# Kernel tuning notes

Measured on AMD Instinct MI355X. Metric: run time of the kernel, lower is better.

Reference implementation:

```python
import jax, jax.numpy as jnp
import numpy as np

B, CIN, CCTX, K, V, T, KS = 8, 512, 512, 64, 256, 1024, 23
EPS = 1e-5


def _bn(z, gamma, beta):
    # train-mode BatchNorm1d over (batch, time) per channel, biased variance
    mean = jnp.mean(z, axis=(0, 2), keepdims=True)
    var = jnp.mean((z - mean) ** 2, axis=(0, 2), keepdims=True)
    return (z - mean) * jax.lax.rsqrt(var + EPS) * gamma[None, :, None] + beta[None, :, None]


def setup_inputs() -> dict:
    key = jax.random.key(0)
    ks = jax.random.split(key, 10)
    x = jax.random.normal(ks[0], (B, CIN, T), dtype=jnp.float32)
    context = jax.random.normal(ks[1], (B, CCTX, T), dtype=jnp.float32)
    Wq = jax.random.normal(ks[2], (K, CIN), dtype=jnp.float32) * (CIN ** -0.5)
    bq = jnp.zeros((K,), dtype=jnp.float32)
    Wk = jax.random.normal(ks[3], (K, CCTX), dtype=jnp.float32) * (CCTX ** -0.5)
    bk = jnp.zeros((K,), dtype=jnp.float32)
    Wv = jax.random.normal(ks[4], (V, CCTX), dtype=jnp.float32) * (CCTX ** -0.5)
    bv = jnp.zeros((V,), dtype=jnp.float32)
    gamma_q = jnp.ones((K,), dtype=jnp.float32)
    beta_q = jnp.zeros((K,), dtype=jnp.float32)
    gamma_v = jnp.ones((V,), dtype=jnp.float32)
    beta_v = jnp.zeros((V,), dtype=jnp.float32)
    pos_w = jax.random.normal(ks[5], (K, KS), dtype=jnp.float32) * (KS ** -0.5)
    pos_b = jnp.zeros((K,), dtype=jnp.float32)
    return {"x": x, "context": context, "Wq": Wq, "bq": bq, "Wk": Wk, "bk": bk,
            "Wv": Wv, "bv": bv, "gamma_q": gamma_q, "beta_q": beta_q,
            "gamma_v": gamma_v, "beta_v": beta_v, "pos_w": pos_w, "pos_b": pos_b}


def reference(x, context, Wq, bq, Wk, bk, Wv, bv,
              gamma_q, beta_q, gamma_v, beta_v, pos_w, pos_b):
    # 1x1 conv1d == channel matmul
    queries = jnp.einsum('bct,kc->bkt', x, Wq) + bq[None, :, None]          # (B,K,T)
    keys = jnp.einsum('bct,kc->bkt', context, Wk) + bk[None, :, None]       # (B,K,T)
    values = jnp.einsum('bct,vc->bvt', context, Wv) + bv[None, :, None]     # (B,V,T)

    norm_keys = jax.nn.softmax(keys, axis=-1)                               # softmax over T
    queries = _bn(queries, gamma_q, beta_q)
    values = _bn(values, gamma_v, beta_v)

    q_t = jnp.transpose(queries, (0, 2, 1))                                 # (B,T,K)
    v_t = jnp.transpose(values, (0, 2, 1))                                  # (B,T,V)

    content_lambda = jnp.einsum('bkt,btv->bkv', norm_keys, v_t)             # (B,K,V)

    # positional conv2d: kernel (K,1,KS,1), padding (KS//2, 0) along T
    lhs = v_t[:, None, :, :]                                                # (B,1,T,V)
    rhs = pos_w[:, None, :, None]                                           # (K,1,KS,1)
    pl = jax.lax.conv_general_dilated(
        lhs, rhs, window_strides=(1, 1),
        padding=[(KS // 2, KS // 2), (0, 0)],
        dimension_numbers=('NCHW', 'OIHW', 'NCHW'))
    pl = pl + pos_b[None, :, None, None]                                    # (B,K,T,V)
    pl = jnp.transpose(pl, (0, 2, 1, 3))                                    # (B,T,K,V)

    content_out = jnp.einsum('btk,bkv->btv', q_t, content_lambda)           # (B,T,V)
    positional_out = jnp.einsum('btk,btkv->btv', q_t, pl)                   # (B,T,V)

    return jnp.transpose(content_out + positional_out, (0, 2, 1))           # (B,V,T)
```

## Files before the change

kernel.cpp:

```cpp
#include <hip/hip_runtime.h>
#include <math.h>

#define B_ 8
#define CIN_ 512
#define K_ 64
#define V_ 256
#define T_ 1024
#define KS_ 23
#define EPS_ 1e-5f
#define NTC_ 8

typedef __attribute__((ext_vector_type(8))) short bf16x8;
typedef __attribute__((ext_vector_type(4))) float f32x4;

__device__ __forceinline__ unsigned short f2bf(float f) {
    union { float f; unsigned u; } x; x.f = f;
    unsigned r = x.u + 0x7fffu + ((x.u >> 16) & 1u);
    return (unsigned short)(r >> 16);
}
__device__ __forceinline__ float bf2f(unsigned short h) {
    union { unsigned u; float f; } x; x.u = ((unsigned)h) << 16;
    return x.f;
}

__device__ __forceinline__ void gload16(const unsigned short* g, unsigned short* l) {
    __builtin_amdgcn_global_load_lds(
        (const __attribute__((address_space(1))) unsigned int*)(const void*)g,
        (__attribute__((address_space(3))) unsigned int*)(void*)l, 16, 0, 0);
}

__global__ __launch_bounds__(256) void prep_kernel(
    const float* __restrict__ x, const float* __restrict__ ctx,
    const float* __restrict__ Wq, const float* __restrict__ Wk,
    const float* __restrict__ Wv,
    unsigned short* __restrict__ xT, unsigned short* __restrict__ cT,
    unsigned short* __restrict__ Wb, float* __restrict__ stat)
{
    __shared__ unsigned short sh[64][72];
    const int tid = threadIdx.x;
    const int id = blockIdx.x;
    if (id < 2048) {
        const int t0 = (id & 15) * 64, c0 = ((id >> 4) & 7) * 64;
        const int z = id >> 7, b = z & 7, which = z >> 3;
        const float* src = which ? ctx : x;
        unsigned short* dst = which ? cT : xT;
        const int cl = tid >> 2, qq = tid & 3;
        const float* row = src + ((size_t)b * CIN_ + c0 + cl) * T_ + t0 + qq * 16;
        #pragma unroll
        for (int u = 0; u < 4; u++) {
            float4 f = *(const float4*)(row + 4 * u);
            sh[qq * 16 + 4 * u + 0][cl] = f2bf(f.x);
            sh[qq * 16 + 4 * u + 1][cl] = f2bf(f.y);
            sh[qq * 16 + 4 * u + 2][cl] = f2bf(f.z);
            sh[qq * 16 + 4 * u + 3][cl] = f2bf(f.w);
        }
        __syncthreads();
        const int tl = tid >> 2;
        unsigned short* orow = dst + ((size_t)b * T_ + t0 + tl) * CIN_ + c0 + qq * 16;
        *(bf16x8*)(orow)     = *(bf16x8*)&sh[tl][qq * 16];
        *(bf16x8*)(orow + 8) = *(bf16x8*)&sh[tl][qq * 16 + 8];
    } else {
        const int wid = id - 2048;
        if (wid == 0) {
            #pragma unroll
            for (int i = 0; i < 3; i++) {
                int idx = tid + i * 256;
                if (idx < 672) ((float4*)stat)[idx] = make_float4(0.f, 0.f, 0.f, 0.f);
            }
        }
        const int i4 = wid * 256 + tid;
        const int n1 = K_ * CIN_ / 4, n2 = 2 * K_ * CIN_ / 4;
        const float* src; int off;
        if (i4 < n1)      { src = Wq; off = i4; }
        else if (i4 < n2) { src = Wk; off = i4 - n1; }
        else              { src = Wv; off = i4 - n2; }
        float4 f = ((const float4*)src)[off];
        ushort4 h;
        h.x = f2bf(f.x); h.y = f2bf(f.y); h.z = f2bf(f.z); h.w = f2bf(f.w);
        *(ushort4*)(Wb + (size_t)i4 * 4) = h;
    }
}

__global__ __launch_bounds__(256) void proj_mfma6(
    const unsigned short* __restrict__ xT, const unsigned short* __restrict__ cT,
    const unsigned short* __restrict__ Wb,
    const float* __restrict__ bq, const float* __restrict__ bk,
    const float* __restrict__ bv,
    float* __restrict__ k_buf, float* __restrict__ v_raw,
    unsigned short* __restrict__ qT, float* __restrict__ stat,
    float* __restrict__ kml)
{
    __shared__ __align__(16) unsigned short SMb[2][12288];

    const int tid = threadIdx.x;
    const int b = blockIdx.z, t0 = blockIdx.x * 128, yb = blockIdx.y;

    const unsigned short* in; const unsigned short* W; const float* bias;
    float* outp = nullptr; int ch0 = 0; float* ssum = nullptr; float* ssq = nullptr;
    if (yb == 0)      { in = xT; W = Wb;             bias = bq;
                        ssum = stat; ssq = stat + 64; ch0 = 0; }
    else if (yb == 1) { in = cT; W = Wb + K_ * CIN_; bias = bk;
                        outp = k_buf + (size_t)b * K_ * T_; }
    else { int m0 = (yb - 2) * 64; in = cT;
           W = Wb + 2 * K_ * CIN_ + (size_t)m0 * CIN_; bias = bv + m0;
           outp = v_raw + ((size_t)b * V_ + m0) * T_;
           ssum = stat + 128; ssq = stat + 384; ch0 = m0; }

    const int lane = tid & 63, w = tid >> 6;
    const int col = lane & 15, quad = lane >> 4;

    const int gW0 = (0 * 4 + w) * 64 + lane, rW0 = gW0 >> 3;
    const int gW1 = (1 * 4 + w) * 64 + lane, rW1 = gW1 >> 3;
    const unsigned short* sW0 = W + (size_t)rW0 * CIN_ + (((gW0 & 7) ^ (rW0 & 7)) * 8);
    const unsigned short* sW1 = W + (size_t)rW1 * CIN_ + (((gW1 & 7) ^ (rW1 & 7)) * 8);

    const int gX0 = (0 * 4 + w) * 64 + lane, rX0 = gX0 >> 3;
    const int gX1 = (1 * 4 + w) * 64 + lane, rX1 = gX1 >> 3;
    const int gX2 = (2 * 4 + w) * 64 + lane, rX2 = gX2 >> 3;
    const int gX3 = (3 * 4 + w) * 64 + lane, rX3 = gX3 >> 3;
    const size_t xbase = (size_t)b * T_ + t0;
    const unsigned short* sX0 = in + (xbase + rX0) * CIN_ + (((gX0 & 7) ^ (rX0 & 7)) * 8);
    const unsigned short* sX1 = in + (xbase + rX1) * CIN_ + (((gX1 & 7) ^ (rX1 & 7)) * 8);
    const unsigned short* sX2 = in + (xbase + rX2) * CIN_ + (((gX2 & 7) ^ (rX2 & 7)) * 8);
    const unsigned short* sX3 = in + (xbase + rX3) * CIN_ + (((gX3 & 7) ^ (rX3 & 7)) * 8);

#define STAGE(P, C0) do { \
    unsigned short* Wt_ = SMb[P]; \
    unsigned short* Xt_ = SMb[P] + 4096; \
    gload16(sW0 + (C0), Wt_ + w * 512); \
    gload16(sW1 + (C0), Wt_ + 2048 + w * 512); \
    gload16(sX0 + (C0), Xt_ + w * 512); \
    gload16(sX1 + (C0), Xt_ + 2048 + w * 512); \
    gload16(sX2 + (C0), Xt_ + 4096 + w * 512); \
    gload16(sX3 + (C0), Xt_ + 6144 + w * 512); \
} while (0)

    f32x4 acc[8];
    #pragma unroll
    for (int j = 0; j < 8; j++) acc[j] = (f32x4){0.f, 0.f, 0.f, 0.f};

    STAGE(0, 0);
    for (int s = 0; s < 8; s++) {
        const int cur = s & 1;
        if (s < 7) {
            STAGE(cur ^ 1, (s + 1) * 64);
            asm volatile("s_waitcnt vmcnt(6)" ::: "memory");
        } else {
            asm volatile("s_waitcnt vmcnt(0)" ::: "memory");
        }
        __builtin_amdgcn_s_barrier();
        __builtin_amdgcn_sched_barrier(0);
        {
            const unsigned short* Wt = SMb[cur];
            const unsigned short* Xt = SMb[cur] + 4096;
            #pragma unroll
            for (int ks = 0; ks < 2; ks++) {
                const int kc = ((ks * 4 + quad) ^ (col & 7)) * 8;
                bf16x8 af = *(bf16x8*)&Wt[(w * 16 + col) * 64 + kc];
                #pragma unroll
                for (int j = 0; j < 8; j++) {
                    bf16x8 bfr = *(bf16x8*)&Xt[(j * 16 + col) * 64 + kc];
                    acc[j] = __builtin_amdgcn_mfma_f32_16x16x32_bf16(af, bfr, acc[j], 0, 0, 0);
                }
            }
        }
        __builtin_amdgcn_sched_barrier(0);
        __builtin_amdgcn_s_barrier();
    }
#undef STAGE

    float bias_v[4], s_[4], sq[4], mr[4], lr[4];
    #pragma unroll
    for (int r = 0; r < 4; r++) {
        bias_v[r] = bias[w * 16 + quad * 4 + r];
        s_[r] = 0.f; sq[r] = 0.f; mr[r] = -1e30f; lr[r] = 0.f;
    }
    unsigned short* SE = SMb[0];
    #pragma unroll
    for (int j = 0; j < 8; j++) {
        float o[4];
        #pragma unroll
        for (int r = 0; r < 4; r++) {
            o[r] = acc[j][r] + bias_v[r];
            s_[r] += o[r]; sq[r] += o[r] * o[r];
        }
        if (yb == 0) {
            ushort4 h;
            h.x = f2bf(o[0]); h.y = f2bf(o[1]); h.z = f2bf(o[2]); h.w = f2bf(o[3]);
            *(ushort4*)&SE[(j * 16 + col) * 72 + w * 16 + quad * 4] = h;
        } else {
            #pragma unroll
            for (int r = 0; r < 4; r++)
                outp[(size_t)(w * 16 + quad * 4 + r) * T_ + t0 + j * 16 + col] = o[r];
            if (yb == 1) {
                #pragma unroll
                for (int r = 0; r < 4; r++) {
                    float mn = fmaxf(mr[r], o[r]);
                    lr[r] = lr[r] * __expf(mr[r] - mn) + __expf(o[r] - mn);
                    mr[r] = mn;
                }
            }
        }
    }
    if (yb == 0) {
        __syncthreads();
        const int tr = tid >> 1, h2 = tid & 1;
        unsigned short* dq = qT + ((size_t)b * T_ + t0 + tr) * K_ + h2 * 32;
        #pragma unroll
        for (int u = 0; u < 4; u++)
            *(bf16x8*)(dq + u * 8) = *(bf16x8*)&SE[tr * 72 + h2 * 32 + u * 8];
    }
    if (yb == 1) {
        #pragma unroll
        for (int r = 0; r < 4; r++) {
            float m = mr[r], l = lr[r];
            #pragma unroll
            for (int off = 1; off < 16; off <<= 1) {
                float mo = __shfl_xor(m, off, 64);
                float lo = __shfl_xor(l, off, 64);
                float mn = fmaxf(m, mo);
                l = l * __expf(m - mn) + lo * __expf(mo - mn);
                m = mn;
            }
            if (col == 0) {
                int row = w * 16 + quad * 4 + r;
                float* p = kml + (((size_t)b * K_ + row) * 8 + (t0 >> 7)) * 2;
                p[0] = m; p[1] = l;
            }
        }
    } else {
        #pragma unroll
        for (int r = 0; r < 4; r++) {
            float sv = s_[r], qv = sq[r];
            #pragma unroll
            for (int off = 1; off < 16; off <<= 1) {
                sv += __shfl_xor(sv, off, 64);
                qv += __shfl_xor(qv, off, 64);
            }
            if (col == 0) {
                int ch = ch0 + w * 16 + quad * 4 + r;
                atomicAdd(&ssum[ch], sv);
                atomicAdd(&ssq[ch], qv);
            }
        }
    }
}

__global__ __launch_bounds__(256) void lambda_kernel5(
    const float* __restrict__ k_buf, const float* __restrict__ v_raw,
    const float* __restrict__ kml, float* __restrict__ clp)
{
    __shared__ __align__(16) float nks[K_][68];
    __shared__ __align__(16) float vls[64][68];
    __shared__ float mrow[64], lrow[64];
    const int tid = threadIdx.x;
    const int b = blockIdx.z, v0 = blockIdx.y * 64, tc = blockIdx.x;

    if (tid < 64) {
        const float2* p = (const float2*)(kml + ((size_t)b * K_ + tid) * 16);
        float m = -1e30f, l = 0.f;
        #pragma unroll
        for (int sgi = 0; sgi < 8; sgi++) {
            float2 ml = p[sgi];
            float mn = fmaxf(m, ml.x);
            l = l * __expf(m - mn) + ml.y * __expf(ml.x - mn);
            m = mn;
        }
        mrow[tid] = m; lrow[tid] = 1.f / l;
    }
    __syncthreads();

    const int r = tid >> 2, q = tid & 3;
    const int tv = tid & 15, tk = tid >> 4;
    float4 acc[4];
    #pragma unroll
    for (int i = 0; i < 4; i++) acc[i] = make_float4(0.f, 0.f, 0.f, 0.f);

    for (int c2 = 0; c2 < 2; c2++) {
        const int t0 = (tc * 2 + c2) * 64;
        if (c2) __syncthreads();
        {
            const float* nrow = k_buf + ((size_t)b * K_ + r) * T_ + t0;
            const float* vrow = v_raw + ((size_t)b * V_ + v0 + r) * T_ + t0;
            const float mr = mrow[r], li = lrow[r];
            #pragma unroll
            for (int i = 0; i < 4; i++) {
                int c4 = q + 4 * i;
                float4 g = *(const float4*)(nrow + 4 * c4);
                g.x = __expf(g.x - mr) * li; g.y = __expf(g.y - mr) * li;
                g.z = __expf(g.z - mr) * li; g.w = __expf(g.w - mr) * li;
                *(float4*)&nks[r][4 * c4] = g;
                float4 h = *(const float4*)(vrow + 4 * c4);
                vls[4 * c4 + 0][r] = h.x; vls[4 * c4 + 1][r] = h.y;
                vls[4 * c4 + 2][r] = h.z; vls[4 * c4 + 3][r] = h.w;
            }
        }
        __syncthreads();
        for (int tt = 0; tt < 16; tt++) {
            float4 w0 = *(float4*)&vls[4 * tt + 0][4 * tv];
            float4 w1 = *(float4*)&vls[4 * tt + 1][4 * tv];
            float4 w2 = *(float4*)&vls[4 * tt + 2][4 * tv];
            float4 w3 = *(float4*)&vls[4 * tt + 3][4 * tv];
            #pragma unroll
            for (int i = 0; i < 4; i++) {
                float4 n = *(float4*)&nks[4 * tk + i][4 * tt];
                acc[i] += w0 * n.x + w1 * n.y + w2 * n.z + w3 * n.w;
            }
        }
    }
    #pragma unroll
    for (int i = 0; i < 4; i++)
        *(float4*)&clp[(((size_t)b * NTC_ + tc) * K_ + 4 * tk + i) * V_ + v0 + 4 * tv] = acc[i];
}

__global__ __launch_bounds__(256) void prep_cl_kernel3(
    const float* __restrict__ clp, const float* __restrict__ stat,
    const float* __restrict__ gq, const float* __restrict__ betaq,
    const float* __restrict__ gv, const float* __restrict__ betav,
    unsigned short* __restrict__ clb2, float* __restrict__ hterm)
{
    __shared__ float qsc[64], qsh[64], red[4][64];
    const int tid = threadIdx.x;
    const int b = blockIdx.y, v0 = blockIdx.x * 64, kz = blockIdx.z;
    const float inv_n = 1.f / (B_ * T_);
    if (tid < 64) {
        float mean = stat[tid] * inv_n;
        float var  = stat[64 + tid] * inv_n - mean * mean;
        float sc = gq[tid] * rsqrtf(var + EPS_);
        qsc[tid] = sc; qsh[tid] = betaq[tid] - mean * sc;
    }
    const int vl = tid & 63, kq = tid >> 6;
    const int c = v0 + vl;
    float vmean = stat[128 + c] * inv_n;
    float vvar  = stat[384 + c] * inv_n - vmean * vmean;
    float vsv = gv[c] * rsqrtf(vvar + EPS_);
    float vhv = betav[c] - vmean * vsv;
    __syncthreads();
    float h = 0.f;
    #pragma unroll
    for (int kk = 0; kk < 4; kk++) {
        int k = kz * 16 + kq * 4 + kk;
        float a = 0.f;
        #pragma unroll
        for (int tc = 0; tc < NTC_; tc++)
            a += clp[(((size_t)b * NTC_ + tc) * K_ + k) * V_ + c];
        float clbv = a * vsv + vhv;
        h += qsh[k] * clbv;
        clb2[((size_t)b * V_ + c) * K_ + k] = f2bf(clbv * qsc[k]);
    }
    red[kq][vl] = h;
    __syncthreads();
    if (tid < 64)
        atomicAdd(&hterm[(size_t)b * V_ + v0 + tid],
                  red[0][tid] + red[1][tid] + red[2][tid] + red[3][tid]);
}

__global__ __launch_bounds__(256) void out_kernel5(
    const unsigned short* __restrict__ qT, const unsigned short* __restrict__ clb2,
    const float* __restrict__ hterm, const float* __restrict__ v_raw,
    const float* __restrict__ stat,
    const float* __restrict__ gq, const float* __restrict__ betaq,
    const float* __restrict__ gv, const float* __restrict__ betav,
    const float* __restrict__ pos_w, const float* __restrict__ pos_b,
    float* __restrict__ out)
{
    __shared__ unsigned short qTt[64][72];
    __shared__ unsigned short clv[64][72];
    __shared__ float vs2T[88][68];
    __shared__ float qpt[64][28];
    __shared__ float pws[64][24];
    __shared__ float qsc[64], qsh[64];
    __shared__ float consts[24];
    __shared__ float hvs[64];
    const int tid = threadIdx.x;
    const int b = blockIdx.z, v0 = blockIdx.y * 64, t0 = blockIdx.x * 64;
    const float inv_n = 1.f / (B_ * T_);

    if (tid < 64) {
        float mean = stat[tid] * inv_n;
        float var  = stat[64 + tid] * inv_n - mean * mean;
        float sc = gq[tid] * rsqrtf(var + EPS_);
        qsc[tid] = sc; qsh[tid] = betaq[tid] - mean * sc;
        hvs[tid] = hterm[(size_t)b * V_ + v0 + tid];
    }
    {
        const int rl = tid >> 2, part = tid & 3;
        const unsigned short* qs = qT + ((size_t)b * T_ + t0 + rl) * K_ + part * 16;
        *(bf16x8*)&qTt[rl][part * 16]     = *(const bf16x8*)(qs);
        *(bf16x8*)&qTt[rl][part * 16 + 8] = *(const bf16x8*)(qs + 8);
        const unsigned short* cs = clb2 + ((size_t)b * V_ + v0 + rl) * K_ + part * 16;
        *(bf16x8*)&clv[rl][part * 16]     = *(const bf16x8*)(cs);
        *(bf16x8*)&clv[rl][part * 16 + 8] = *(const bf16x8*)(cs + 8);
    }
    {
        const int vl = tid >> 2, qq = tid & 3;
        const int c = v0 + vl;
        float vmean = stat[128 + c] * inv_n;
        float vvar  = stat[384 + c] * inv_n - vmean * vmean;
        float vsv = gv[c] * rsqrtf(vvar + EPS_);
        float vhv = betav[c] - vmean * vsv;
        const float* vrow = v_raw + ((size_t)b * V_ + c) * T_;
        #pragma unroll
        for (int i = 0; i < 22; i++) {
            int cc = qq + 4 * i;
            if (cc < 86) {
                int t = t0 + cc - 11;
                vs2T[cc][vl] = (t >= 0 && t < T_) ? vrow[t] * vsv + vhv : 0.f;
            }
        }
    }
    __syncthreads();

    for (int idx = tid; idx < K_ * 24; idx += 256) {
        int k = idx / 24, s = idx % 24;
        pws[k][s] = qsc[k] * (s < KS_ ? pos_w[k * KS_ + s] : pos_b[k]);
    }
    if (tid < 24) {
        float cs = 0.f;
        for (int k = 0; k < K_; k++)
            cs += qsh[k] * (tid < KS_ ? pos_w[k * KS_ + tid] : pos_b[k]);
        consts[tid] = cs;
    }
    __syncthreads();

    {
        const int t = tid >> 2, sg = tid & 3, s0 = sg * 6;
        float a[6];
        #pragma unroll
        for (int u = 0; u < 6; u++) a[u] = consts[s0 + u];
        #pragma unroll
        for (int kb = 0; kb < 8; kb++) {
            bf16x8 qv = *(bf16x8*)&qTt[t][kb * 8];
            #pragma unroll
            for (int j = 0; j < 8; j++) {
                float q = bf2f((unsigned short)qv[j]);
                #pragma unroll
                for (int u = 0; u < 6; u++) a[u] += q * pws[kb * 8 + j][s0 + u];
            }
        }
        #pragma unroll
        for (int u = 0; u < 6; u++) qpt[t][s0 + u] = a[u];
    }
    __syncthreads();

    const int lane = tid & 63, w = tid >> 6;
    const int col = lane & 15, quad = lane >> 4;

    f32x4 acc[4];
    #pragma unroll
    for (int tf = 0; tf < 4; tf++) acc[tf] = (f32x4){0.f, 0.f, 0.f, 0.f};

    #pragma unroll
    for (int ks = 0; ks < 2; ks++) {
        const int kc = ks * 32 + quad * 8;
        bf16x8 af = *(bf16x8*)&clv[w * 16 + col][kc];
        #pragma unroll
        for (int tf = 0; tf < 4; tf++) {
            bf16x8 bq = *(bf16x8*)&qTt[tf * 16 + col][kc];
            acc[tf] = __builtin_amdgcn_mfma_f32_16x16x32_bf16(af, bq, acc[tf], 0, 0, 0);
        }
    }

    const int vb = w * 16 + quad * 4;
    float4 hv4 = *(float4*)&hvs[vb];
    #pragma unroll
    for (int tf = 0; tf < 4; tf++) {
        const int lt = tf * 16 + col;
        float qv[24];
        #pragma unroll
        for (int u = 0; u < 6; u++)
            *(float4*)&qv[4 * u] = *(float4*)&qpt[lt][4 * u];
        float4 a; a.x = acc[tf][0]; a.y = acc[tf][1]; a.z = acc[tf][2]; a.w = acc[tf][3];
        #pragma unroll
        for (int s = 0; s < KS_; s++) {
            float4 wv = *(float4*)&vs2T[lt + s][vb];
            a.x += qv[s] * wv.x; a.y += qv[s] * wv.y;
            a.z += qv[s] * wv.z; a.w += qv[s] * wv.w;
        }
        float base = qv[23];
        a.x += base + hv4.x; a.y += base + hv4.y;
        a.z += base + hv4.z; a.w += base + hv4.w;
        float* ap = (float*)&a;
        #pragma unroll
        for (int r = 0; r < 4; r++)
            out[((size_t)b * V_ + v0 + vb + r) * T_ + t0 + lt] = ap[r];
    }
}

extern "C" void kernel_launch(void* const* d_in, const int* in_sizes, int n_in,
                              void* d_out, int out_size, void* d_ws, size_t ws_size,
                              hipStream_t stream)
{
    const float* x     = (const float*)d_in[0];
    const float* ctx   = (const float*)d_in[1];
    const float* Wq    = (const float*)d_in[2];
    const float* bq    = (const float*)d_in[3];
    const float* Wk    = (const float*)d_in[4];
    const float* bk    = (const float*)d_in[5];
    const float* Wv    = (const float*)d_in[6];
    const float* bv    = (const float*)d_in[7];
    const float* gq    = (const float*)d_in[8];
    const float* betaq = (const float*)d_in[9];
    const float* gv    = (const float*)d_in[10];
    const float* betav = (const float*)d_in[11];
    const float* pos_w = (const float*)d_in[12];
    const float* pos_b = (const float*)d_in[13];
    float* out = (float*)d_out;

    float* ws    = (float*)d_ws;
    float* k_buf = ws;
    float* v_raw = k_buf + (size_t)B_ * K_ * T_;
    float* clp   = v_raw + (size_t)B_ * V_ * T_;
    float* stat  = clp + (size_t)B_ * NTC_ * K_ * V_;
    float* hterm = stat + 640;
    float* kml   = hterm + (size_t)B_ * V_;
    unsigned short* xT   = (unsigned short*)(kml + (size_t)B_ * K_ * 16);
    unsigned short* cT   = xT + (size_t)B_ * T_ * CIN_;
    unsigned short* Wb   = cT + (size_t)B_ * T_ * CIN_;
    unsigned short* qT   = Wb + (size_t)(2 * K_ + V_) * CIN_;
    unsigned short* clb2 = qT + (size_t)B_ * T_ * K_;

    prep_kernel<<<dim3(2048 + 192), 256, 0, stream>>>(
        x, ctx, Wq, Wk, Wv, xT, cT, Wb, stat);
    proj_mfma6<<<dim3(T_ / 128, 6, B_), 256, 0, stream>>>(
        xT, cT, Wb, bq, bk, bv, k_buf, v_raw, qT, stat, kml);
    lambda_kernel5<<<dim3(NTC_, V_ / 64, B_), 256, 0, stream>>>(k_buf, v_raw, kml, clp);
    prep_cl_kernel3<<<dim3(V_ / 64, B_, 4), 256, 0, stream>>>(
        clp, stat, gq, betaq, gv, betav, clb2, hterm);
    out_kernel5<<<dim3(T_ / 64, V_ / 64, B_), 256, 0, stream>>>(
        qT, clb2, hterm, v_raw, stat, gq, betaq, gv, betav, pos_w, pos_b, out);
}
```

Baseline: 148.0 us.

## Fuse content-lambda reduction and BN folding into output kernel

Removes the separate prep_cl kernel. Each output block now sums the per-chunk partial lambdas from clp, applies the value and query BN scales, and builds the bf16 lambda tile and h-term in shared memory using warp shuffles. This drops one launch plus the clb2/hterm global round trip and the atomics. The cost is that the lambda reduction is recomputed by each of the 16 t-blocks sharing a (b, v) tile, which adds redundant global reads of clp (8 partials × 64×64 floats per block).

```diff
diff --git a/kernel.cpp b/kernel.cpp
--- a/kernel.cpp
+++ b/kernel.cpp
@@ -61,13 +61,8 @@
         *(bf16x8*)(orow + 8) = *(bf16x8*)&sh[tl][qq * 16 + 8];
     } else {
         const int wid = id - 2048;
-        if (wid == 0) {
-            #pragma unroll
-            for (int i = 0; i < 3; i++) {
-                int idx = tid + i * 256;
-                if (idx < 672) ((float4*)stat)[idx] = make_float4(0.f, 0.f, 0.f, 0.f);
-            }
-        }
+        if (wid == 0 && tid < 160)
+            ((float4*)stat)[tid] = make_float4(0.f, 0.f, 0.f, 0.f);
         const int i4 = wid * 256 + tid;
         const int n1 = K_ * CIN_ / 4, n2 = 2 * K_ * CIN_ / 4;
         const float* src; int off;
@@ -313,52 +308,9 @@
         *(float4*)&clp[(((size_t)b * NTC_ + tc) * K_ + 4 * tk + i) * V_ + v0 + 4 * tv] = acc[i];
 }
 
-__global__ __launch_bounds__(256) void prep_cl_kernel3(
-    const float* __restrict__ clp, const float* __restrict__ stat,
-    const float* __restrict__ gq, const float* __restrict__ betaq,
-    const float* __restrict__ gv, const float* __restrict__ betav,
-    unsigned short* __restrict__ clb2, float* __restrict__ hterm)
-{
-    __shared__ float qsc[64], qsh[64], red[4][64];
-    const int tid = threadIdx.x;
-    const int b = blockIdx.y, v0 = blockIdx.x * 64, kz = blockIdx.z;
-    const float inv_n = 1.f / (B_ * T_);
-    if (tid < 64) {
-        float mean = stat[tid] * inv_n;
-        float var  = stat[64 + tid] * inv_n - mean * mean;
-        float sc = gq[tid] * rsqrtf(var + EPS_);
-        qsc[tid] = sc; qsh[tid] = betaq[tid] - mean * sc;
-    }
-    const int vl = tid & 63, kq = tid >> 6;
-    const int c = v0 + vl;
-    float vmean = stat[128 + c] * inv_n;
-    float vvar  = stat[384 + c] * inv_n - vmean * vmean;
-    float vsv = gv[c] * rsqrtf(vvar + EPS_);
-    float vhv = betav[c] - vmean * vsv;
-    __syncthreads();
-    float h = 0.f;
-    #pragma unroll
-    for (int kk = 0; kk < 4; kk++) {
-        int k = kz * 16 + kq * 4 + kk;
-        float a = 0.f;
-        #pragma unroll
-        for (int tc = 0; tc < NTC_; tc++)
-            a += clp[(((size_t)b * NTC_ + tc) * K_ + k) * V_ + c];
-        float clbv = a * vsv + vhv;
-        h += qsh[k] * clbv;
-        clb2[((size_t)b * V_ + c) * K_ + k] = f2bf(clbv * qsc[k]);
-    }
-    red[kq][vl] = h;
-    __syncthreads();
-    if (tid < 64)
-        atomicAdd(&hterm[(size_t)b * V_ + v0 + tid],
-                  red[0][tid] + red[1][tid] + red[2][tid] + red[3][tid]);
-}
-
-__global__ __launch_bounds__(256) void out_kernel5(
-    const unsigned short* __restrict__ qT, const unsigned short* __restrict__ clb2,
-    const float* __restrict__ hterm, const float* __restrict__ v_raw,
-    const float* __restrict__ stat,
+__global__ __launch_bounds__(256) void out_kernel6(
+    const unsigned short* __restrict__ qT, const float* __restrict__ clp,
+    const float* __restrict__ v_raw, const float* __restrict__ stat,
     const float* __restrict__ gq, const float* __restrict__ betaq,
     const float* __restrict__ gv, const float* __restrict__ betav,
     const float* __restrict__ pos_w, const float* __restrict__ pos_b,
@@ -369,9 +321,10 @@
     __shared__ float vs2T[88][68];
     __shared__ float qpt[64][28];
     __shared__ float pws[64][24];
-    __shared__ float qsc[64], qsh[64];
+    __shared__ float qsc[64], qsh[64], vsc[64], vsh[64];
     __shared__ float consts[24];
     __shared__ float hvs[64];
+    __shared__ float hred[4][4][16];
     const int tid = threadIdx.x;
     const int b = blockIdx.z, v0 = blockIdx.y * 64, t0 = blockIdx.x * 64;
     const float inv_n = 1.f / (B_ * T_);
@@ -381,16 +334,17 @@
         float var  = stat[64 + tid] * inv_n - mean * mean;
         float sc = gq[tid] * rsqrtf(var + EPS_);
         qsc[tid] = sc; qsh[tid] = betaq[tid] - mean * sc;
-        hvs[tid] = hterm[(size_t)b * V_ + v0 + tid];
+        int c = v0 + tid;
+        float vmean = stat[128 + c] * inv_n;
+        float vvar  = stat[384 + c] * inv_n - vmean * vmean;
+        float vs = gv[c] * rsqrtf(vvar + EPS_);
+        vsc[tid] = vs; vsh[tid] = betav[c] - vmean * vs;
     }
     {
         const int rl = tid >> 2, part = tid & 3;
         const unsigned short* qs = qT + ((size_t)b * T_ + t0 + rl) * K_ + part * 16;
         *(bf16x8*)&qTt[rl][part * 16]     = *(const bf16x8*)(qs);
         *(bf16x8*)&qTt[rl][part * 16 + 8] = *(const bf16x8*)(qs + 8);
-        const unsigned short* cs = clb2 + ((size_t)b * V_ + v0 + rl) * K_ + part * 16;
-        *(bf16x8*)&clv[rl][part * 16]     = *(const bf16x8*)(cs);
-        *(bf16x8*)&clv[rl][part * 16 + 8] = *(const bf16x8*)(cs + 8);
     }
     {
         const int vl = tid >> 2, qq = tid & 3;
@@ -409,8 +363,36 @@
             }
         }
     }
+    const int kk = tid >> 2, cq = (tid & 3) * 16;
+    float4 a0 = make_float4(0.f,0.f,0.f,0.f), a1 = a0, a2 = a0, a3 = a0;
+    #pragma unroll
+    for (int tc = 0; tc < NTC_; tc++) {
+        const float4* p = (const float4*)(clp + (((size_t)b * NTC_ + tc) * K_ + kk) * V_ + v0 + cq);
+        a0.x += p[0].x; a0.y += p[0].y; a0.z += p[0].z; a0.w += p[0].w;
+        a1.x += p[1].x; a1.y += p[1].y; a1.z += p[1].z; a1.w += p[1].w;
+        a2.x += p[2].x; a2.y += p[2].y; a2.z += p[2].z; a2.w += p[2].w;
+        a3.x += p[3].x; a3.y += p[3].y; a3.z += p[3].z; a3.w += p[3].w;
+    }
     __syncthreads();
 
+    {
+        const int lane = tid & 63, w = tid >> 6;
+        float av[16];
+        *(float4*)&av[0] = a0; *(float4*)&av[4] = a1;
+        *(float4*)&av[8] = a2; *(float4*)&av[12] = a3;
+        const float qscv = qsc[kk], qshv = qsh[kk];
+        #pragma unroll
+        for (int i = 0; i < 16; i++) {
+            float clbv = av[i] * vsc[cq + i] + vsh[cq + i];
+            clv[cq + i][kk] = f2bf(clbv * qscv);
+            float h = qshv * clbv;
+            h += __shfl_xor(h, 4, 64);
+            h += __shfl_xor(h, 8, 64);
+            h += __shfl_xor(h, 16, 64);
+            h += __shfl_xor(h, 32, 64);
+            if (lane < 4) hred[w][lane][i] = h;
+        }
+    }
     for (int idx = tid; idx < K_ * 24; idx += 256) {
         int k = idx / 24, s = idx % 24;
         pws[k][s] = qsc[k] * (s < KS_ ? pos_w[k * KS_ + s] : pos_b[k]);
@@ -423,6 +405,9 @@
     }
     __syncthreads();
 
+    if (tid < 64)
+        hvs[tid] = hred[0][tid >> 4][tid & 15] + hred[1][tid >> 4][tid & 15]
+                 + hred[2][tid >> 4][tid & 15] + hred[3][tid >> 4][tid & 15];
     {
         const int t = tid >> 2, sg = tid & 3, s0 = sg * 6;
         float a[6];
@@ -512,21 +497,17 @@
     float* v_raw = k_buf + (size_t)B_ * K_ * T_;
     float* clp   = v_raw + (size_t)B_ * V_ * T_;
     float* stat  = clp + (size_t)B_ * NTC_ * K_ * V_;
-    float* hterm = stat + 640;
-    float* kml   = hterm + (size_t)B_ * V_;
+    float* kml   = stat + 640;
     unsigned short* xT   = (unsigned short*)(kml + (size_t)B_ * K_ * 16);
     unsigned short* cT   = xT + (size_t)B_ * T_ * CIN_;
     unsigned short* Wb   = cT + (size_t)B_ * T_ * CIN_;
     unsigned short* qT   = Wb + (size_t)(2 * K_ + V_) * CIN_;
-    unsigned short* clb2 = qT + (size_t)B_ * T_ * K_;
 
     prep_kernel<<<dim3(2048 + 192), 256, 0, stream>>>(
         x, ctx, Wq, Wk, Wv, xT, cT, Wb, stat);
     proj_mfma6<<<dim3(T_ / 128, 6, B_), 256, 0, stream>>>(
         xT, cT, Wb, bq, bk, bv, k_buf, v_raw, qT, stat, kml);
     lambda_kernel5<<<dim3(NTC_, V_ / 64, B_), 256, 0, stream>>>(k_buf, v_raw, kml, clp);
-    prep_cl_kernel3<<<dim3(V_ / 64, B_, 4), 256, 0, stream>>>(
-        clp, stat, gq, betaq, gv, betav, clb2, hterm);
-    out_kernel5<<<dim3(T_ / 64, V_ / 64, B_), 256, 0, stream>>>(
-        qT, clb2, hterm, v_raw, stat, gq, betaq, gv, betav, pos_w, pos_b, out);
-}
+    out_kernel6<<<dim3(T_ / 64, V_ / 64, B_), 256, 0, stream>>>(
+        qT, clp, v_raw, stat, gq, betaq, gv, betav, pos_w, pos_b, out);
+}
```

After: 153.5 us. 1.04x slower.
